# Optimization experiments

Hardware: AMD Instinct MI355X
Metric: run time of the kernel (lower is better)

The kernel has to match this reference:

```python
import jax, jax.numpy as jnp
import numpy as np

VOCAB_LIST = np.array([16384, 2048, 256], dtype=np.int64)
SIZES = VOCAB_LIST + 1                       # +1 level-mask token per level
LEVEL_ENDS = jnp.asarray(np.cumsum(SIZES))   # [3] cumulative vocab ends
MASK_TOKENS = LEVEL_ENDS - 1                 # level mask token ids
TOTAL_V = int(SIZES.sum())                   # 18691
N_LAYER, N_EMBD, N_HEAD = 4, 1024, 16
HEAD_DIM = N_EMBD // N_HEAD
FF = 4 * N_EMBD
MEMORY_SPAN = 256
SOFTCAP = 30.0


def rms_norm(x):
    return x * jax.lax.rsqrt(jnp.mean(x * x, axis=-1, keepdims=True) + 1e-6)


def rotary(x):
    # x: [B, S, H, D]; half-split rotation as in modded-nanogpt
    S, D = x.shape[1], x.shape[-1]
    half = D // 2
    inv_freq = 1.0 / (10000.0 ** (jnp.arange(half, dtype=jnp.float32) / half))
    freqs = jnp.outer(jnp.arange(S, dtype=jnp.float32), inv_freq)  # [S, half]
    cos = jnp.cos(freqs)[None, :, None, :]
    sin = jnp.sin(freqs)[None, :, None, :]
    x1, x2 = x[..., :half], x[..., half:]
    return jnp.concatenate([x1 * cos + x2 * sin, -x1 * sin + x2 * cos], axis=-1)


def build_mask(levels):
    # keep kv if causal AND (kv is a higher-level 'global' token OR within recent window)
    S = levels.shape[1]
    q = jnp.arange(S)[:, None]
    k = jnp.arange(S)[None, :]
    causal = q >= k
    recent = (q - k) <= MEMORY_SPAN
    higher = (levels > 0)[:, None, :]                 # [B,1,S]
    return causal[None] & (higher | recent[None])     # [B,S,S]


def forward(idx, target, wte, lambdas, lamb, wq, wk, wv, wo, w1, w2, lm_head):
    B, S = idx.shape
    levels = jnp.searchsorted(LEVEL_ENDS, idx, side='right')   # infer_level
    mask = build_mask(levels)[:, None]                         # [B,1,S,S]
    x = rms_norm(wte[idx])
    x0 = x
    v1 = None
    for i in range(N_LAYER):
        xr = lambdas[i, 0] * x + lambdas[i, 1] * x0
        h = rms_norm(xr)
        q = (h @ wq[i].T).reshape(B, S, N_HEAD, HEAD_DIM)
        k = (h @ wk[i].T).reshape(B, S, N_HEAD, HEAD_DIM)
        v = (h @ wv[i].T).reshape(B, S, N_HEAD, HEAD_DIM)
        if v1 is None:
            v1 = v                                  # value residual from layer 0
        v = (1.0 - lamb[i]) * v + lamb[i] * v1
        q = rotary(rms_norm(q))                     # QK-norm then rotary
        k = rotary(rms_norm(k))
        scores = jnp.einsum('bqhd,bkhd->bhqk', q, k) / jnp.sqrt(jnp.float32(HEAD_DIM))
        scores = jnp.where(mask, scores, -jnp.inf)
        attn = jax.nn.softmax(scores, axis=-1)
        y = jnp.einsum('bhqk,bkhd->bqhd', attn, v).reshape(B, S, N_EMBD)
        x = xr + y @ wo[i].T
        m = rms_norm(x)
        x = x + (jax.nn.relu(m @ w1[i].T) ** 2) @ w2[i].T   # ReLU^2 MLP
    x = rms_norm(x)
    logits = x @ lm_head.T
    logits = SOFTCAP * jnp.tanh(logits / SOFTCAP)
    logp = jax.nn.log_softmax(logits.astype(jnp.float32), axis=-1)
    loss = -jnp.take_along_axis(logp, target[..., None].astype(jnp.int32), axis=-1)[..., 0]
    loss = jnp.where(jnp.isin(target, MASK_TOKENS), 0.0, loss)
    return loss


def setup_inputs() -> dict:
    key = jax.random.key(0)
    ks = jax.random.split(key, 12)
    B, S, D, V, F, L = 2, 2048, N_EMBD, TOTAL_V, FF, N_LAYER
    s = 0.02
    return {
        'idx': jax.random.randint(ks[0], (B, S), 0, V, dtype=jnp.int32),
        'target': jax.random.randint(ks[1], (B, S), 0, V, dtype=jnp.int32),
        'wte': jax.random.normal(ks[2], (V, D), dtype=jnp.float32),
        'lambdas': jnp.tile(jnp.array([1.0, 0.0], dtype=jnp.float32), (L, 1)),
        'lamb': jnp.full((L,), 0.5, dtype=jnp.float32),
        'wq': jax.random.normal(ks[3], (L, D, D), dtype=jnp.float32) * s,
        'wk': jax.random.normal(ks[4], (L, D, D), dtype=jnp.float32) * s,
        'wv': jax.random.normal(ks[5], (L, D, D), dtype=jnp.float32) * s,
        'wo': jax.random.normal(ks[6], (L, D, D), dtype=jnp.float32) * s,
        'w1': jax.random.normal(ks[7], (L, F, D), dtype=jnp.float32) * s,
        'w2': jax.random.normal(ks[8], (L, D, F), dtype=jnp.float32) * s,
        'lm_head': jax.random.normal(ks[9], (V, D), dtype=jnp.float32) * 0.01,
    }


def reference(idx, target, wte, lambdas, lamb, wq, wk, wv, wo, w1, w2, lm_head):
    return forward(idx, target, wte, lambdas, lamb, wq, wk, wv, wo, w1, w2, lm_head)
```

## Files before the change

### kernel.cpp

```cpp
#include <hip/hip_runtime.h>
#include <hip/hip_bf16.h>

#define TT 4096
#define SS 2048
#define BBATCH 2
#define DM 1024
#define NH 16
#define HD 64
#define FFD 4096
#define NL 4
#define VV 18691
#define VP 18816
#define APITCH 72
#define LCHUNK 6272
#define SENT 0x3FFFFFFF

typedef __bf16 bf16x8 __attribute__((ext_vector_type(8)));
typedef float f32x4 __attribute__((ext_vector_type(4)));
typedef const __attribute__((address_space(1))) void* gas_t;
typedef __attribute__((address_space(3))) void* las_t;

__device__ __forceinline__ float bfb2f(unsigned short u) {
    union { unsigned int i; float f; } x;
    x.i = ((unsigned int)u) << 16;
    return x.f;
}
__device__ __forceinline__ unsigned short f2bfb(float f) {
    union { float f; unsigned int i; } x;
    x.f = f;
    unsigned int r = 0x7fffu + ((x.i >> 16) & 1u);
    x.i += r;
    return (unsigned short)(x.i >> 16);
}

__device__ __forceinline__ float wave_sum(float v) {
#pragma unroll
    for (int o = 32; o; o >>= 1) v += __shfl_xor(v, o, 64);
    return v;
}

__device__ __forceinline__ float block_sum256(float v) {
    __shared__ float sb[4];
    v = wave_sum(v);
    int wid = threadIdx.x >> 6;
    if ((threadIdx.x & 63) == 0) sb[wid] = v;
    __syncthreads();
    float t = sb[0] + sb[1] + sb[2] + sb[3];
    __syncthreads();
    return t;
}

__global__ __launch_bounds__(256) void cvtw_kernel(const float* __restrict__ src,
                                                   unsigned short* __restrict__ dst, int n)
{
    int i = (blockIdx.x * 256 + threadIdx.x) * 4;
    if (i >= n) return;
    float4 f = *reinterpret_cast<const float4*>(src + i);
    ushort4 u;
    u.x = f2bfb(f.x); u.y = f2bfb(f.y); u.z = f2bfb(f.z); u.w = f2bfb(f.w);
    *reinterpret_cast<ushort4*>(dst + i) = u;
}

__global__ __launch_bounds__(256) void cvtpad_kernel(const float* __restrict__ src,
                                                     unsigned short* __restrict__ dst,
                                                     int nreal, int ntot)
{
    int i = (blockIdx.x * 256 + threadIdx.x) * 4;
    if (i >= ntot) return;
    ushort4 u = {0, 0, 0, 0};
    if (i < nreal) {
        float4 f = *reinterpret_cast<const float4*>(src + i);
        u.x = f2bfb(f.x); u.y = f2bfb(f.y); u.z = f2bfb(f.z); u.w = f2bfb(f.w);
    }
    *reinterpret_cast<ushort4*>(dst + i) = u;
}

__global__ __launch_bounds__(256) void embed_kernel(
    const int* __restrict__ idx, const float* __restrict__ wte,
    float* __restrict__ x, unsigned short* __restrict__ x0, int* __restrict__ levels)
{
    int t = blockIdx.x;
    int id = idx[t];
    const float* row = wte + (size_t)id * DM;
    float4 v = *reinterpret_cast<const float4*>(row + threadIdx.x * 4);
    float ss = v.x * v.x + v.y * v.y + v.z * v.z + v.w * v.w;
    float tot = block_sum256(ss);
    float rs = rsqrtf(tot / (float)DM + 1e-6f);
    float4 o;
    o.x = v.x * rs; o.y = v.y * rs; o.z = v.z * rs; o.w = v.w * rs;
    size_t off = (size_t)t * DM + threadIdx.x * 4;
    *reinterpret_cast<float4*>(x + off) = o;
    ushort4 ub;
    ub.x = f2bfb(o.x); ub.y = f2bfb(o.y); ub.z = f2bfb(o.z); ub.w = f2bfb(o.w);
    *reinterpret_cast<ushort4*>(x0 + off) = ub;
    if (threadIdx.x == 0) levels[t] = (id >= 16385) + (id >= 18434);
}

__global__ __launch_bounds__(256) void pack_kernel(
    const int* __restrict__ levels, int* __restrict__ gpos, int* __restrict__ nbuf)
{
    int b = blockIdx.x;
    const int* lv = levels + b * SS;
    int* gp = gpos + b * SS;
    __shared__ int wsum[4];
    __shared__ int base;
    if (threadIdx.x == 0) base = 0;
    __syncthreads();
    int lane = threadIdx.x & 63, w = threadIdx.x >> 6;
    for (int c = 0; c < SS; c += 256) {
        int s = c + threadIdx.x;
        int flag = (lv[s] > 0) ? 1 : 0;
        unsigned long long mask = __ballot(flag);
        int pre = __popcll(mask & ((1ull << lane) - 1ull));
        int wtot = __popcll(mask);
        if (lane == 0) wsum[w] = wtot;
        __syncthreads();
        int woff = 0;
#pragma unroll
        for (int i = 0; i < 4; ++i) if (i < w) woff += wsum[i];
        int tot = wsum[0] + wsum[1] + wsum[2] + wsum[3];
        int mybase = base;
        if (flag) gp[mybase + woff + pre] = s;
        __syncthreads();
        if (threadIdx.x == 0) base += tot;
        __syncthreads();
    }
    int nb = base;
    int nbp = (nb + 63) & ~63;
    for (int i = nb + threadIdx.x; i < SS; i += 256) gp[i] = SENT;
    if (threadIdx.x == 0) { nbuf[b] = nb; nbuf[BBATCH + b] = nbp; }
}

__global__ __launch_bounds__(64) void gather_kernel(
    const unsigned short* __restrict__ kb, const unsigned short* __restrict__ vb,
    const int* __restrict__ gpos, const int* __restrict__ nbuf,
    unsigned short* __restrict__ kp, unsigned short* __restrict__ vp)
{
    int b = blockIdx.x >> 11;
    int j = blockIdx.x & (SS - 1);
    if (j >= nbuf[BBATCH + b]) return;
    int pos = gpos[b * SS + j];
    int lane = threadIdx.x;
    size_t dst = ((size_t)b * SS + j) * DM + lane * 16;
    if (pos < SS) {
        size_t src = ((size_t)b * SS + pos) * DM + lane * 16;
        *reinterpret_cast<uint4*>(kp + dst) = *reinterpret_cast<const uint4*>(kb + src);
        *reinterpret_cast<uint4*>(kp + dst + 8) = *reinterpret_cast<const uint4*>(kb + src + 8);
        *reinterpret_cast<uint4*>(vp + dst) = *reinterpret_cast<const uint4*>(vb + src);
        *reinterpret_cast<uint4*>(vp + dst + 8) = *reinterpret_cast<const uint4*>(vb + src + 8);
    } else {
        uint4 z = {0, 0, 0, 0};
        *reinterpret_cast<uint4*>(kp + dst) = z;
        *reinterpret_cast<uint4*>(kp + dst + 8) = z;
        *reinterpret_cast<uint4*>(vp + dst) = z;
        *reinterpret_cast<uint4*>(vp + dst + 8) = z;
    }
}

__global__ __launch_bounds__(256) void mixnorm_kernel(
    float* __restrict__ x, const unsigned short* __restrict__ x0,
    const float* __restrict__ lam2, unsigned short* __restrict__ out)
{
    int t = blockIdx.x;
    size_t off = (size_t)t * DM + threadIdx.x * 4;
    float4 xv = *reinterpret_cast<const float4*>(x + off);
    float l0 = lam2[0], l1 = lam2[1];
    ushort4 u = *reinterpret_cast<const ushort4*>(x0 + off);
    float4 r;
    r.x = l0 * xv.x + l1 * bfb2f(u.x);
    r.y = l0 * xv.y + l1 * bfb2f(u.y);
    r.z = l0 * xv.z + l1 * bfb2f(u.z);
    r.w = l0 * xv.w + l1 * bfb2f(u.w);
    float ss = r.x * r.x + r.y * r.y + r.z * r.z + r.w * r.w;
    float tot = block_sum256(ss);
    float rs = rsqrtf(tot / (float)DM + 1e-6f);
    *reinterpret_cast<float4*>(x + off) = r;
    ushort4 ob;
    ob.x = f2bfb(r.x * rs); ob.y = f2bfb(r.y * rs);
    ob.z = f2bfb(r.z * rs); ob.w = f2bfb(r.w * rs);
    *reinterpret_cast<ushort4*>(out + off) = ob;
}

__global__ __launch_bounds__(256) void norm_kernel(
    const float* __restrict__ x, unsigned short* __restrict__ out)
{
    int t = blockIdx.x;
    size_t off = (size_t)t * DM + threadIdx.x * 4;
    float4 r = *reinterpret_cast<const float4*>(x + off);
    float ss = r.x * r.x + r.y * r.y + r.z * r.z + r.w * r.w;
    float tot = block_sum256(ss);
    float rs = rsqrtf(tot / (float)DM + 1e-6f);
    ushort4 ob;
    ob.x = f2bfb(r.x * rs); ob.y = f2bfb(r.y * rs);
    ob.z = f2bfb(r.z * rs); ob.w = f2bfb(r.w * rs);
    *reinterpret_cast<ushort4*>(out + off) = ob;
}

template <int EPI>
__global__ __launch_bounds__(256) void gemm_bb(
    const unsigned short* __restrict__ A, const unsigned short* __restrict__ Bw,
    unsigned short* __restrict__ Cb, float* __restrict__ Cf,
    unsigned short* __restrict__ Kb, unsigned short* __restrict__ Vb,
    int NX, int K, int ldC)
{
    __shared__ unsigned short As[128 * 64];
    __shared__ unsigned short Bs[128 * 64];

    int nwg = gridDim.x;
    int orig = blockIdx.x;
    int qq = nwg >> 3, rr = nwg & 7;
    int xcd = orig & 7, rem = orig >> 3;
    int wg = (xcd < rr ? xcd * (qq + 1) : rr * (qq + 1) + (xcd - rr) * qq) + rem;
    int bx = wg % NX, by = wg / NX;
    int m0 = by * 128, n0 = bx * 128;

    int tid = threadIdx.x, lane = tid & 63, w = tid >> 6;
    int wr = w >> 1, wc = w & 1;
    int rsub = lane >> 3, sl = lane & 7;
    int ssrc = sl ^ rsub;
    int fr = lane & 15, fh = lane >> 4;

    size_t arow[4], brow[4];
#pragma unroll
    for (int i = 0; i < 4; ++i) {
        int c = 4 * w + i;
        arow[i] = (size_t)(m0 + 8 * c + rsub) * K + ssrc * 8;
        brow[i] = (size_t)(n0 + 8 * c + rsub) * K + ssrc * 8;
    }

    f32x4 acc[4][4];
#pragma unroll
    for (int m = 0; m < 4; ++m)
#pragma unroll
        for (int n = 0; n < 4; ++n) acc[m][n] = 0.0f;

    int NT = K >> 6;
    for (int kt = 0; kt < NT; ++kt) {
        int kb = kt * 64;
#pragma unroll
        for (int i = 0; i < 4; ++i) {
            __builtin_amdgcn_global_load_lds((gas_t)(const void*)(A + arow[i] + kb),
                                             (las_t)(void*)(&As[(4 * w + i) * 512]), 16, 0, 0);
            __builtin_amdgcn_global_load_lds((gas_t)(const void*)(Bw + brow[i] + kb),
                                             (las_t)(void*)(&Bs[(4 * w + i) * 512]), 16, 0, 0);
        }
        __syncthreads();
#pragma unroll
        for (int kk = 0; kk < 2; ++kk) {
            int slot = kk * 4 + fh;
            bf16x8 af[4], bfv[4];
#pragma unroll
            for (int m = 0; m < 4; ++m) {
                int row = wr * 64 + m * 16 + fr;
                af[m] = *reinterpret_cast<const bf16x8*>(&As[row * 64 + ((slot ^ (row & 7)) << 3)]);
            }
#pragma unroll
            for (int n = 0; n < 4; ++n) {
                int row = wc * 64 + n * 16 + fr;
                bfv[n] = *reinterpret_cast<const bf16x8*>(&Bs[row * 64 + ((slot ^ (row & 7)) << 3)]);
            }
#pragma unroll
            for (int m = 0; m < 4; ++m)
#pragma unroll
                for (int n = 0; n < 4; ++n)
                    acc[m][n] = __builtin_amdgcn_mfma_f32_16x16x32_bf16(af[m], bfv[n], acc[m][n], 0, 0, 0);
        }
        __syncthreads();
    }

    int rb = m0 + wr * 64 + fh * 4;
    int cb = n0 + wc * 64 + fr;
    unsigned short* outp = Cb;
    if constexpr (EPI == 3) {
        int mat = n0 >> 10;
        outp = (mat == 0) ? Cb : ((mat == 1) ? Kb : Vb);
    }
#pragma unroll
    for (int n = 0; n < 4; ++n) {
        int gc = cb + n * 16;
#pragma unroll
        for (int m = 0; m < 4; ++m) {
#pragma unroll
            for (int j = 0; j < 4; ++j) {
                int gr = rb + m * 16 + j;
                float val = acc[m][n][j];
                if constexpr (EPI == 0) {
                    Cb[(size_t)gr * ldC + gc] = f2bfb(val);
                } else if constexpr (EPI == 1) {
                    float rl = fmaxf(val, 0.0f);
                    Cb[(size_t)gr * ldC + gc] = f2bfb(rl * rl);
                } else if constexpr (EPI == 2) {
                    size_t o = (size_t)gr * ldC + gc;
                    Cf[o] = Cf[o] + val;
                } else {
                    outp[(size_t)gr * DM + (gc & 1023)] = f2bfb(val);
                }
            }
        }
    }
}

template <int EPI>
__global__ __launch_bounds__(256) void gemm_bb64(
    const unsigned short* __restrict__ A, const unsigned short* __restrict__ Bw,
    unsigned short* __restrict__ Cb, float* __restrict__ Cf,
    int NX, int K, int ldC)
{
    __shared__ unsigned short As[64 * 64];
    __shared__ unsigned short Bs[128 * 64];

    int nwg = gridDim.x;
    int orig = blockIdx.x;
    int qq = nwg >> 3, rr = nwg & 7;
    int xcd = orig & 7, rem = orig >> 3;
    int wg = (xcd < rr ? xcd * (qq + 1) : rr * (qq + 1) + (xcd - rr) * qq) + rem;
    int bx = wg % NX, by = wg / NX;
    int m0 = by * 64, n0 = bx * 128;

    int tid = threadIdx.x, lane = tid & 63, w = tid >> 6;
    int wr = w >> 1, wc = w & 1;
    int rsub = lane >> 3, sl = lane & 7;
    int ssrc = sl ^ rsub;
    int fr = lane & 15, fh = lane >> 4;

    size_t arow[2], brow[4];
#pragma unroll
    for (int i = 0; i < 2; ++i) {
        int c = 2 * w + i;
        arow[i] = (size_t)(m0 + 8 * c + rsub) * K + ssrc * 8;
    }
#pragma unroll
    for (int i = 0; i < 4; ++i) {
        int c = 4 * w + i;
        brow[i] = (size_t)(n0 + 8 * c + rsub) * K + ssrc * 8;
    }

    f32x4 acc[2][4];
#pragma unroll
    for (int m = 0; m < 2; ++m)
#pragma unroll
        for (int n = 0; n < 4; ++n) acc[m][n] = 0.0f;

    int NT = K >> 6;
    for (int kt = 0; kt < NT; ++kt) {
        int kb = kt * 64;
#pragma unroll
        for (int i = 0; i < 2; ++i)
            __builtin_amdgcn_global_load_lds((gas_t)(const void*)(A + arow[i] + kb),
                                             (las_t)(void*)(&As[(2 * w + i) * 512]), 16, 0, 0);
#pragma unroll
        for (int i = 0; i < 4; ++i)
            __builtin_amdgcn_global_load_lds((gas_t)(const void*)(Bw + brow[i] + kb),
                                             (las_t)(void*)(&Bs[(4 * w + i) * 512]), 16, 0, 0);
        __syncthreads();
#pragma unroll
        for (int kk = 0; kk < 2; ++kk) {
            int slot = kk * 4 + fh;
            bf16x8 af[2], bfv[4];
#pragma unroll
            for (int m = 0; m < 2; ++m) {
                int row = wr * 32 + m * 16 + fr;
                af[m] = *reinterpret_cast<const bf16x8*>(&As[row * 64 + ((slot ^ (row & 7)) << 3)]);
            }
#pragma unroll
            for (int n = 0; n < 4; ++n) {
                int row = wc * 64 + n * 16 + fr;
                bfv[n] = *reinterpret_cast<const bf16x8*>(&Bs[row * 64 + ((slot ^ (row & 7)) << 3)]);
            }
#pragma unroll
            for (int m = 0; m < 2; ++m)
#pragma unroll
                for (int n = 0; n < 4; ++n)
                    acc[m][n] = __builtin_amdgcn_mfma_f32_16x16x32_bf16(af[m], bfv[n], acc[m][n], 0, 0, 0);
        }
        __syncthreads();
    }

    int rb = m0 + wr * 32 + fh * 4;
    int cb = n0 + wc * 64 + fr;
#pragma unroll
    for (int n = 0; n < 4; ++n) {
        int gc = cb + n * 16;
#pragma unroll
        for (int m = 0; m < 2; ++m) {
#pragma unroll
            for (int j = 0; j < 4; ++j) {
                int gr = rb + m * 16 + j;
                float val = acc[m][n][j];
                if constexpr (EPI == 0) {
                    Cb[(size_t)gr * ldC + gc] = f2bfb(val);
                } else if constexpr (EPI == 1) {
                    float rl = fmaxf(val, 0.0f);
                    Cb[(size_t)gr * ldC + gc] = f2bfb(rl * rl);
                } else {
                    size_t o = (size_t)gr * ldC + gc;
                    Cf[o] = Cf[o] + val;
                }
            }
        }
    }
}

__global__ void vcopy_kernel(const unsigned short* __restrict__ v, unsigned short* __restrict__ v1)
{
    int i = blockIdx.x * 256 + threadIdx.x;
    reinterpret_cast<ushort4*>(v1)[i] = reinterpret_cast<const ushort4*>(v)[i];
}

__global__ void vmix_kernel(unsigned short* __restrict__ v, const unsigned short* __restrict__ v1,
                            const float* __restrict__ lamb)
{
    int i = blockIdx.x * 256 + threadIdx.x;
    float la = *lamb;
    ushort4 a = reinterpret_cast<const ushort4*>(v)[i];
    ushort4 b = reinterpret_cast<const ushort4*>(v1)[i];
    ushort4 o;
    o.x = f2bfb((1.0f - la) * bfb2f(a.x) + la * bfb2f(b.x));
    o.y = f2bfb((1.0f - la) * bfb2f(a.y) + la * bfb2f(b.y));
    o.z = f2bfb((1.0f - la) * bfb2f(a.z) + la * bfb2f(b.z));
    o.w = f2bfb((1.0f - la) * bfb2f(a.w) + la * bfb2f(b.w));
    reinterpret_cast<ushort4*>(v)[i] = o;
}

__global__ __launch_bounds__(256) void rope_kernel(unsigned short* __restrict__ q,
                                                   unsigned short* __restrict__ k)
{
    int wid = threadIdx.x >> 6, lane = threadIdx.x & 63;
    int id = blockIdx.x * 4 + wid;
    unsigned short* p = blockIdx.y ? k : q;
    int t = id >> 4, h = id & 15;
    int s = t & (SS - 1);
    size_t off = (size_t)t * DM + h * HD + lane;
    float val = bfb2f(p[off]);
    float ss = wave_sum(val * val);
    float rs = rsqrtf(ss / (float)HD + 1e-6f);
    float nv = val * rs;
    float other = __shfl_xor(nv, 32, 64);
    int j = lane & 31;
    float invf = exp2f(-(float)j * 0.41524101186092025f);
    float fr = (float)s * invf;
    float sn, cs;
    sincosf(fr, &sn, &cs);
    float outv = (lane < 32) ? (nv * cs + other * sn) : (nv * cs - other * sn);
    p[off] = f2bfb(outv);
}

__global__ __launch_bounds__(256) void attn_mfma_kernel(
    const unsigned short* __restrict__ q, const unsigned short* __restrict__ k,
    const unsigned short* __restrict__ v,
    const unsigned short* __restrict__ kp, const unsigned short* __restrict__ vp,
    const int* __restrict__ gpos, const int* __restrict__ nbuf,
    unsigned short* __restrict__ y)
{
    __shared__ unsigned short Qs[64][APITCH];
    __shared__ unsigned short Ks[64][APITCH];
    __shared__ unsigned short Vt[64][APITCH];
    __shared__ unsigned short Ps[64][APITCH];
    __shared__ int posS[64];

    int bh = blockIdx.x;
    int b = bh >> 4, h = bh & 15;
    int q0 = blockIdx.y * 64;
    size_t base = (size_t)b * SS * DM + h * HD;
    int tid = threadIdx.x;
    int lane = tid & 63, w = tid >> 6;
    int srow = tid >> 2, sc = tid & 3;

    {
        const unsigned short* src = q + base + (size_t)(q0 + srow) * DM;
        *reinterpret_cast<uint4*>(&Qs[srow][sc * 8]) = *reinterpret_cast<const uint4*>(src + sc * 8);
        *reinterpret_cast<uint4*>(&Qs[srow][(sc + 4) * 8]) = *reinterpret_cast<const uint4*>(src + (sc + 4) * 8);
    }
    __syncthreads();

    int fr = lane & 15, fc = (lane >> 4) * 8;
    int rj = (lane >> 4) * 4;

    bf16x8 qa[2];
    qa[0] = *reinterpret_cast<const bf16x8*>(&Qs[w * 16 + fr][fc]);
    qa[1] = *reinterpret_cast<const bf16x8*>(&Qs[w * 16 + fr][32 + fc]);

    float mreg[4], lreg[4];
    f32x4 yacc[4];
#pragma unroll
    for (int j = 0; j < 4; ++j) { mreg[j] = -1e30f; lreg[j] = 0.0f; yacc[j] = 0.0f; }

    int nbp = nbuf[BBATCH + b];

    int t0 = (q0 >= 256) ? ((q0 - 256) >> 6) : 0;
    int t1 = q0 >> 6;
    for (int pass = 0; pass < 2; ++pass) {
        int kt_begin = (pass == 0) ? t0 : 0;
        int kt_end = (pass == 0) ? (t1 + 1) : (nbp >> 6);
        for (int kt = kt_begin; kt < kt_end; ++kt) {
            int k0 = kt * 64;
            if (pass == 1) {
                if (gpos[b * SS + k0] > q0 - 194) break;
            }
            __syncthreads();
            {
                const unsigned short* ksrc = (pass == 0) ? (k + base) : (kp + base);
                const unsigned short* vsrc = (pass == 0) ? (v + base) : (vp + base);
                size_t goff = (size_t)(k0 + srow) * DM;
                uint4 kv0 = *reinterpret_cast<const uint4*>(ksrc + goff + sc * 8);
                uint4 kv1 = *reinterpret_cast<const uint4*>(ksrc + goff + (sc + 4) * 8);
                *reinterpret_cast<uint4*>(&Ks[srow][sc * 8]) = kv0;
                *reinterpret_cast<uint4*>(&Ks[srow][(sc + 4) * 8]) = kv1;
                uint4 vv0 = *reinterpret_cast<const uint4*>(vsrc + goff + sc * 8);
                uint4 vv1 = *reinterpret_cast<const uint4*>(vsrc + goff + (sc + 4) * 8);
                const unsigned short* e0 = reinterpret_cast<const unsigned short*>(&vv0);
                const unsigned short* e1 = reinterpret_cast<const unsigned short*>(&vv1);
#pragma unroll
                for (int i = 0; i < 8; ++i) Vt[sc * 8 + i][srow] = e0[i];
#pragma unroll
                for (int i = 0; i < 8; ++i) Vt[(sc + 4) * 8 + i][srow] = e1[i];
                if (pass == 1 && tid < 64) posS[tid] = gpos[b * SS + k0 + tid];
            }
            __syncthreads();

            f32x4 sacc[4];
#pragma unroll
            for (int n = 0; n < 4; ++n) {
                bf16x8 kb0 = *reinterpret_cast<const bf16x8*>(&Ks[n * 16 + fr][fc]);
                bf16x8 kb1 = *reinterpret_cast<const bf16x8*>(&Ks[n * 16 + fr][32 + fc]);
                f32x4 a = {0.0f, 0.0f, 0.0f, 0.0f};
                a = __builtin_amdgcn_mfma_f32_16x16x32_bf16(qa[0], kb0, a, 0, 0, 0);
                a = __builtin_amdgcn_mfma_f32_16x16x32_bf16(qa[1], kb1, a, 0, 0, 0);
                sacc[n] = a;
            }

            float sm[4][4];
            float cm[4] = {-1e30f, -1e30f, -1e30f, -1e30f};
#pragma unroll
            for (int n = 0; n < 4; ++n) {
                int kg = (pass == 0) ? (k0 + n * 16 + fr) : posS[n * 16 + fr];
#pragma unroll
                for (int j = 0; j < 4; ++j) {
                    int qg = q0 + w * 16 + rj + j;
                    bool valid = (pass == 0) ? ((kg <= qg) && (qg - kg <= 256))
                                             : (kg < qg - 256);
                    float s = valid ? sacc[n][j] * 0.125f : -1e30f;
                    sm[n][j] = s;
                    cm[j] = fmaxf(cm[j], s);
                }
            }
#pragma unroll
            for (int j = 0; j < 4; ++j) {
                cm[j] = fmaxf(cm[j], __shfl_xor(cm[j], 1, 64));
                cm[j] = fmaxf(cm[j], __shfl_xor(cm[j], 2, 64));
                cm[j] = fmaxf(cm[j], __shfl_xor(cm[j], 4, 64));
                cm[j] = fmaxf(cm[j], __shfl_xor(cm[j], 8, 64));
            }
            float sj[4], ps[4];
#pragma unroll
            for (int j = 0; j < 4; ++j) {
                float nm = fmaxf(mreg[j], cm[j]);
                sj[j] = __expf(mreg[j] - nm);
                mreg[j] = nm;
                ps[j] = 0.0f;
            }
#pragma unroll
            for (int n = 0; n < 4; ++n) {
#pragma unroll
                for (int j = 0; j < 4; ++j) {
                    float p = (sm[n][j] > -1e29f) ? __expf(sm[n][j] - mreg[j]) : 0.0f;
                    Ps[w * 16 + rj + j][n * 16 + fr] = f2bfb(p);
                    ps[j] += p;
                }
            }
#pragma unroll
            for (int j = 0; j < 4; ++j) {
                float t = ps[j];
                t += __shfl_xor(t, 1, 64); t += __shfl_xor(t, 2, 64);
                t += __shfl_xor(t, 4, 64); t += __shfl_xor(t, 8, 64);
                lreg[j] = lreg[j] * sj[j] + t;
            }
#pragma unroll
            for (int n = 0; n < 4; ++n)
#pragma unroll
                for (int j = 0; j < 4; ++j) yacc[n][j] *= sj[j];

            bf16x8 pa0 = *reinterpret_cast<const bf16x8*>(&Ps[w * 16 + fr][fc]);
            bf16x8 pa1 = *reinterpret_cast<const bf16x8*>(&Ps[w * 16 + fr][32 + fc]);
#pragma unroll
            for (int n = 0; n < 4; ++n) {
                bf16x8 vb0 = *reinterpret_cast<const bf16x8*>(&Vt[n * 16 + fr][fc]);
                bf16x8 vb1 = *reinterpret_cast<const bf16x8*>(&Vt[n * 16 + fr][32 + fc]);
                yacc[n] = __builtin_amdgcn_mfma_f32_16x16x32_bf16(pa0, vb0, yacc[n], 0, 0, 0);
                yacc[n] = __builtin_amdgcn_mfma_f32_16x16x32_bf16(pa1, vb1, yacc[n], 0, 0, 0);
            }
        }
    }

    float inv[4];
#pragma unroll
    for (int j = 0; j < 4; ++j) inv[j] = 1.0f / lreg[j];
#pragma unroll
    for (int n = 0; n < 4; ++n) {
#pragma unroll
        for (int j = 0; j < 4; ++j) {
            int qg = q0 + w * 16 + rj + j;
            y[base + (size_t)qg * DM + n * 16 + fr] = f2bfb(yacc[n][j] * inv[j]);
        }
    }
}

__global__ __launch_bounds__(256) void loss_part_kernel(
    const unsigned short* __restrict__ logits, const int* __restrict__ target,
    float* __restrict__ mbuf, float* __restrict__ lbuf, float* __restrict__ zbuf,
    float* __restrict__ out, int c0, int cn, int last)
{
    int t = blockIdx.x;
    const unsigned short* row = logits + (size_t)t * cn;
    int tg = target[t];
    int tl = tg - c0;
    int lim = min(cn, VV - c0);
    float m = -1e30f, l = 0.0f, ztg = 0.0f;
    for (int i = threadIdx.x; i < lim; i += 256) {
        float z = bfb2f(row[i]);
        z = 30.0f * tanhf(z * (1.0f / 30.0f));
        if (i == tl) ztg = z;
        if (z > m) {
            l = l * __expf(m - z) + 1.0f;
            m = z;
        } else {
            l += __expf(z - m);
        }
    }
    __shared__ float ms[256], ls[256];
    __shared__ float zs;
    if (threadIdx.x == 0) zs = 0.0f;
    ms[threadIdx.x] = m;
    ls[threadIdx.x] = l;
    __syncthreads();
    if (tl >= 0 && tl < lim && threadIdx.x == (tl & 255)) zs = ztg;
    for (int s2 = 128; s2 > 0; s2 >>= 1) {
        __syncthreads();
        if (threadIdx.x < s2) {
            float m2 = ms[threadIdx.x + s2], l2 = ls[threadIdx.x + s2];
            float m1 = ms[threadIdx.x], l1 = ls[threadIdx.x];
            float mm = fmaxf(m1, m2);
            ls[threadIdx.x] = l1 * __expf(m1 - mm) + l2 * __expf(m2 - mm);
            ms[threadIdx.x] = mm;
        }
    }
    __syncthreads();
    if (threadIdx.x == 0) {
        float cmv = ms[0], clv = ls[0], czv = zs;
        float nm, nl, nz;
        if (c0 == 0) {
            nm = cmv; nl = clv; nz = czv;
        } else {
            float pm = mbuf[t], pl = lbuf[t];
            nm = fmaxf(pm, cmv);
            nl = pl * __expf(pm - nm) + clv * __expf(cmv - nm);
            nz = zbuf[t] + czv;
        }
        if (last) {
            float lse = nm + logf(nl);
            bool masked = (tg == 16384) || (tg == 18433) || (tg == 18690);
            out[t] = masked ? 0.0f : (lse - nz);
        } else {
            mbuf[t] = nm; lbuf[t] = nl; zbuf[t] = nz;
        }
    }
}

extern "C" void kernel_launch(void* const* d_in, const int* in_sizes, int n_in,
                              void* d_out, int out_size, void* d_ws, size_t ws_size,
                              hipStream_t stream)
{
    const int* idx = (const int*)d_in[0];
    const int* target = (const int*)d_in[1];
    const float* wte = (const float*)d_in[2];
    const float* lambdas = (const float*)d_in[3];
    const float* lamb = (const float*)d_in[4];
    const float* wq = (const float*)d_in[5];
    const float* wk = (const float*)d_in[6];
    const float* wv = (const float*)d_in[7];
    const float* wo = (const float*)d_in[8];
    const float* w1 = (const float*)d_in[9];
    const float* w2 = (const float*)d_in[10];
    const float* lm_head = (const float*)d_in[11];
    float* out = (float*)d_out;

    char* ws = (char*)d_ws;
    const size_t MB = (size_t)1 << 20;
    float* x            = (float*)(ws);
    unsigned short* x0  = (unsigned short*)(ws + 16 * MB);
    unsigned short* nrm = (unsigned short*)(ws + 24 * MB);
    unsigned short* qb  = (unsigned short*)(ws + 32 * MB);
    unsigned short* kb  = (unsigned short*)(ws + 40 * MB);
    unsigned short* vb  = (unsigned short*)(ws + 48 * MB);
    unsigned short* v1b = (unsigned short*)(ws + 56 * MB);
    unsigned short* yb  = (unsigned short*)(ws + 64 * MB);
    unsigned short* hid = (unsigned short*)(ws + 72 * MB);
    unsigned short* kp  = (unsigned short*)(ws + 72 * MB);
    unsigned short* vp  = (unsigned short*)(ws + 80 * MB);
    int* levels         = (int*)(ws + 104 * MB);
    int* gpos           = (int*)(ws + 104 * MB + 64 * 1024);
    int* nbuf           = (int*)(ws + 104 * MB + 128 * 1024);
    float* mbuf         = (float*)(ws + 104 * MB + 256 * 1024);
    float* lbuf         = mbuf + TT;
    float* zbuf         = lbuf + TT;
    unsigned short* wqkvb = (unsigned short*)(ws + 105 * MB);
    unsigned short* wob = (unsigned short*)(ws + 129 * MB);
    unsigned short* w1b = (unsigned short*)(ws + 137 * MB);
    unsigned short* w2b = (unsigned short*)(ws + 169 * MB);
    unsigned short* lmb = (unsigned short*)(ws + 201 * MB);
    unsigned short* lchunk = qb;
    bool cvt = ws_size >= 238 * MB;

    if (cvt) {
        int n1 = DM * DM;
        int nff = NL * FFD * DM;
        for (int i = 0; i < NL; ++i) {
            cvtw_kernel<<<n1 / 1024, 256, 0, stream>>>(wq + (size_t)i * n1, wqkvb + ((size_t)i * 3 + 0) * n1, n1);
            cvtw_kernel<<<n1 / 1024, 256, 0, stream>>>(wk + (size_t)i * n1, wqkvb + ((size_t)i * 3 + 1) * n1, n1);
            cvtw_kernel<<<n1 / 1024, 256, 0, stream>>>(wv + (size_t)i * n1, wqkvb + ((size_t)i * 3 + 2) * n1, n1);
        }
        cvtw_kernel<<<NL * n1 / 1024, 256, 0, stream>>>(wo, wob, NL * n1);
        cvtw_kernel<<<nff / 1024, 256, 0, stream>>>(w1, w1b, nff);
        cvtw_kernel<<<nff / 1024, 256, 0, stream>>>(w2, w2b, nff);
        cvtpad_kernel<<<(VP * DM) / 1024, 256, 0, stream>>>(lm_head, lmb, VV * DM, VP * DM);
    }

    embed_kernel<<<TT, 256, 0, stream>>>(idx, wte, x, x0, levels);
    pack_kernel<<<BBATCH, 256, 0, stream>>>(levels, gpos, nbuf);

    for (int i = 0; i < NL; ++i) {
        mixnorm_kernel<<<TT, 256, 0, stream>>>(x, x0, lambdas + 2 * i, nrm);
        if (cvt) {
            gemm_bb<3><<<768, 256, 0, stream>>>(nrm, wqkvb + (size_t)i * 3 * DM * DM,
                                                qb, nullptr, kb, vb, 24, DM, DM);
        }
        if (i == 0)
            vcopy_kernel<<<TT * DM / 1024, 256, 0, stream>>>(vb, v1b);
        else
            vmix_kernel<<<TT * DM / 1024, 256, 0, stream>>>(vb, v1b, lamb + i);
        rope_kernel<<<dim3(TT * NH / 4, 2), 256, 0, stream>>>(qb, kb);
        gather_kernel<<<BBATCH * SS, 64, 0, stream>>>(kb, vb, gpos, nbuf, kp, vp);
        attn_mfma_kernel<<<dim3(BBATCH * NH, SS / 64), 256, 0, stream>>>(qb, kb, vb, kp, vp, gpos, nbuf, yb);
        if (cvt) {
            gemm_bb64<2><<<512, 256, 0, stream>>>(yb, wob + (size_t)i * DM * DM, nullptr, x, 8, DM, DM);
            norm_kernel<<<TT, 256, 0, stream>>>(x, nrm);
            gemm_bb<1><<<1024, 256, 0, stream>>>(nrm, w1b + (size_t)i * FFD * DM, hid, nullptr, nullptr, nullptr, 32, DM, FFD);
            gemm_bb64<2><<<512, 256, 0, stream>>>(hid, w2b + (size_t)i * DM * FFD, nullptr, x, 8, FFD, DM);
        }
    }

    norm_kernel<<<TT, 256, 0, stream>>>(x, nrm);
    for (int c = 0; c < 3; ++c) {
        gemm_bb<0><<<(LCHUNK / 128) * 32, 256, 0, stream>>>(
            nrm, lmb + (size_t)c * LCHUNK * DM, lchunk, nullptr, nullptr, nullptr, LCHUNK / 128, DM, LCHUNK);
        loss_part_kernel<<<TT, 256, 0, stream>>>(lchunk, target, mbuf, lbuf, zbuf,
                                                 out, c * LCHUNK, LCHUNK, c == 2);
    }
}
```

Before: 1.498 ms.

## Fuse value-residual mix into QKV epilogue, split-K residual GEMMs, fast softcap

The value-residual copy and mix now happen inside the QKV GEMM epilogue, which removes two elementwise kernels and their extra passes over the value tensor. The Wo and W2 residual GEMMs use a two-way split-K with atomicAdd into the fp32 residual, doubling the number of workgroups to 1024. The softcap tanh in the loss kernel is replaced by an exp-based formula. In exchange, atomics add contention, the summation order becomes nondeterministic, and the softcap may differ slightly in rounding.

```diff
diff --git a/kernel.cpp b/kernel.cpp
--- a/kernel.cpp
+++ b/kernel.cpp
@@ -201,6 +201,8 @@
     const unsigned short* __restrict__ A, const unsigned short* __restrict__ Bw,
     unsigned short* __restrict__ Cb, float* __restrict__ Cf,
     unsigned short* __restrict__ Kb, unsigned short* __restrict__ Vb,
+    const unsigned short* __restrict__ V1in, unsigned short* __restrict__ V1out,
+    const float* __restrict__ lambp,
     int NX, int K, int ldC)
 {
     __shared__ unsigned short As[128 * 64];
@@ -271,9 +273,13 @@
     int rb = m0 + wr * 64 + fh * 4;
     int cb = n0 + wc * 64 + fr;
     unsigned short* outp = Cb;
+    bool vmat = false;
+    float la = 0.0f;
     if constexpr (EPI == 3) {
         int mat = n0 >> 10;
         outp = (mat == 0) ? Cb : ((mat == 1) ? Kb : Vb);
+        vmat = (mat == 2);
+        if (vmat && !V1out) la = *lambp;
     }
 #pragma unroll
     for (int n = 0; n < 4; ++n) {
@@ -293,14 +299,26 @@
                     size_t o = (size_t)gr * ldC + gc;
                     Cf[o] = Cf[o] + val;
                 } else {
-                    outp[(size_t)gr * DM + (gc & 1023)] = f2bfb(val);
+                    size_t o = (size_t)gr * DM + (gc & 1023);
+                    if (vmat) {
+                        unsigned short bv = f2bfb(val);
+                        if (V1out) {
+                            outp[o] = bv;
+                            V1out[o] = bv;
+                        } else {
+                            float mixed = (1.0f - la) * bfb2f(bv) + la * bfb2f(V1in[o]);
+                            outp[o] = f2bfb(mixed);
+                        }
+                    } else {
+                        outp[o] = f2bfb(val);
+                    }
                 }
             }
         }
     }
 }
 
-template <int EPI>
+template <int EPI, int KS>
 __global__ __launch_bounds__(256) void gemm_bb64(
     const unsigned short* __restrict__ A, const unsigned short* __restrict__ Bw,
     unsigned short* __restrict__ Cb, float* __restrict__ Cf,
@@ -314,8 +332,13 @@
     int qq = nwg >> 3, rr = nwg & 7;
     int xcd = orig & 7, rem = orig >> 3;
     int wg = (xcd < rr ? xcd * (qq + 1) : rr * (qq + 1) + (xcd - rr) * qq) + rem;
-    int bx = wg % NX, by = wg / NX;
+    int per = nwg / KS;
+    int ks = wg / per;
+    int rem2 = wg % per;
+    int bx = rem2 % NX, by = rem2 / NX;
     int m0 = by * 64, n0 = bx * 128;
+    int KSUB = K / KS;
+    int kbase = ks * KSUB;
 
     int tid = threadIdx.x, lane = tid & 63, w = tid >> 6;
     int wr = w >> 1, wc = w & 1;
@@ -341,9 +364,9 @@
 #pragma unroll
         for (int n = 0; n < 4; ++n) acc[m][n] = 0.0f;
 
-    int NT = K >> 6;
+    int NT = KSUB >> 6;
     for (int kt = 0; kt < NT; ++kt) {
-        int kb = kt * 64;
+        int kb = kbase + kt * 64;
 #pragma unroll
         for (int i = 0; i < 2; ++i)
             __builtin_amdgcn_global_load_lds((gas_t)(const void*)(A + arow[i] + kb),
@@ -394,32 +417,15 @@
                     Cb[(size_t)gr * ldC + gc] = f2bfb(rl * rl);
                 } else {
                     size_t o = (size_t)gr * ldC + gc;
-                    Cf[o] = Cf[o] + val;
+                    if constexpr (KS == 1) {
+                        Cf[o] = Cf[o] + val;
+                    } else {
+                        atomicAdd(&Cf[o], val);
+                    }
                 }
             }
         }
     }
-}
-
-__global__ void vcopy_kernel(const unsigned short* __restrict__ v, unsigned short* __restrict__ v1)
-{
-    int i = blockIdx.x * 256 + threadIdx.x;
-    reinterpret_cast<ushort4*>(v1)[i] = reinterpret_cast<const ushort4*>(v)[i];
-}
-
-__global__ void vmix_kernel(unsigned short* __restrict__ v, const unsigned short* __restrict__ v1,
-                            const float* __restrict__ lamb)
-{
-    int i = blockIdx.x * 256 + threadIdx.x;
-    float la = *lamb;
-    ushort4 a = reinterpret_cast<const ushort4*>(v)[i];
-    ushort4 b = reinterpret_cast<const ushort4*>(v1)[i];
-    ushort4 o;
-    o.x = f2bfb((1.0f - la) * bfb2f(a.x) + la * bfb2f(b.x));
-    o.y = f2bfb((1.0f - la) * bfb2f(a.y) + la * bfb2f(b.y));
-    o.z = f2bfb((1.0f - la) * bfb2f(a.z) + la * bfb2f(b.z));
-    o.w = f2bfb((1.0f - la) * bfb2f(a.w) + la * bfb2f(b.w));
-    reinterpret_cast<ushort4*>(v)[i] = o;
 }
 
 __global__ __launch_bounds__(256) void rope_kernel(unsigned short* __restrict__ q,
@@ -605,6 +611,13 @@
     }
 }
 
+__device__ __forceinline__ float softcap(float z) {
+    float a = z * (2.0f / 30.0f);
+    a = fminf(fmaxf(a, -30.0f), 30.0f);
+    float t = __expf(a);
+    return 30.0f * __fdividef(t - 1.0f, t + 1.0f);
+}
+
 __global__ __launch_bounds__(256) void loss_part_kernel(
     const unsigned short* __restrict__ logits, const int* __restrict__ target,
     float* __restrict__ mbuf, float* __restrict__ lbuf, float* __restrict__ zbuf,
@@ -617,8 +630,7 @@
     int lim = min(cn, VV - c0);
     float m = -1e30f, l = 0.0f, ztg = 0.0f;
     for (int i = threadIdx.x; i < lim; i += 256) {
-        float z = bfb2f(row[i]);
-        z = 30.0f * tanhf(z * (1.0f / 30.0f));
+        float z = softcap(bfb2f(row[i]));
         if (i == tl) ztg = z;
         if (z > m) {
             l = l * __expf(m - z) + 1.0f;
@@ -731,28 +743,30 @@
     for (int i = 0; i < NL; ++i) {
         mixnorm_kernel<<<TT, 256, 0, stream>>>(x, x0, lambdas + 2 * i, nrm);
         if (cvt) {
-            gemm_bb<3><<<768, 256, 0, stream>>>(nrm, wqkvb + (size_t)i * 3 * DM * DM,
-                                                qb, nullptr, kb, vb, 24, DM, DM);
-        }
-        if (i == 0)
-            vcopy_kernel<<<TT * DM / 1024, 256, 0, stream>>>(vb, v1b);
-        else
-            vmix_kernel<<<TT * DM / 1024, 256, 0, stream>>>(vb, v1b, lamb + i);
+            if (i == 0)
+                gemm_bb<3><<<768, 256, 0, stream>>>(nrm, wqkvb + (size_t)i * 3 * DM * DM,
+                                                    qb, nullptr, kb, vb, nullptr, v1b, nullptr, 24, DM, DM);
+            else
+                gemm_bb<3><<<768, 256, 0, stream>>>(nrm, wqkvb + (size_t)i * 3 * DM * DM,
+                                                    qb, nullptr, kb, vb, v1b, nullptr, lamb + i, 24, DM, DM);
+        }
         rope_kernel<<<dim3(TT * NH / 4, 2), 256, 0, stream>>>(qb, kb);
         gather_kernel<<<BBATCH * SS, 64, 0, stream>>>(kb, vb, gpos, nbuf, kp, vp);
         attn_mfma_kernel<<<dim3(BBATCH * NH, SS / 64), 256, 0, stream>>>(qb, kb, vb, kp, vp, gpos, nbuf, yb);
         if (cvt) {
-            gemm_bb64<2><<<512, 256, 0, stream>>>(yb, wob + (size_t)i * DM * DM, nullptr, x, 8, DM, DM);
+            gemm_bb64<2, 2><<<1024, 256, 0, stream>>>(yb, wob + (size_t)i * DM * DM, nullptr, x, 8, DM, DM);
             norm_kernel<<<TT, 256, 0, stream>>>(x, nrm);
-            gemm_bb<1><<<1024, 256, 0, stream>>>(nrm, w1b + (size_t)i * FFD * DM, hid, nullptr, nullptr, nullptr, 32, DM, FFD);
-            gemm_bb64<2><<<512, 256, 0, stream>>>(hid, w2b + (size_t)i * DM * FFD, nullptr, x, 8, FFD, DM);
+            gemm_bb<1><<<1024, 256, 0, stream>>>(nrm, w1b + (size_t)i * FFD * DM, hid, nullptr,
+                                                 nullptr, nullptr, nullptr, nullptr, nullptr, 32, DM, FFD);
+            gemm_bb64<2, 2><<<1024, 256, 0, stream>>>(hid, w2b + (size_t)i * DM * FFD, nullptr, x, 8, FFD, DM);
         }
     }
 
     norm_kernel<<<TT, 256, 0, stream>>>(x, nrm);
     for (int c = 0; c < 3; ++c) {
         gemm_bb<0><<<(LCHUNK / 128) * 32, 256, 0, stream>>>(
-            nrm, lmb + (size_t)c * LCHUNK * DM, lchunk, nullptr, nullptr, nullptr, LCHUNK / 128, DM, LCHUNK);
+            nrm, lmb + (size_t)c * LCHUNK * DM, lchunk, nullptr,
+            nullptr, nullptr, nullptr, nullptr, nullptr, LCHUNK / 128, DM, LCHUNK);
         loss_part_kernel<<<TT, 256, 0, stream>>>(lchunk, target, mbuf, lbuf, zbuf,
                                                  out, c * LCHUNK, LCHUNK, c == 2);
     }
```

Result: slower. 1.576 ms (+5.2%).
